# Kernel optimization log

Measured on AMD Instinct MI355X. Metric: run time of the kernel, lower is better.

The kernel has to match this reference:

```python
import jax, jax.numpy as jnp
import numpy as np

C = 64          # channels (init arg)
G = 64          # input latent grid side -> output grid side 2G = 128
S = 2 * G + 2   # padded side for injective key encoding (coords shifted by +1)
N_IN = 60_000


def _encode(coords):
    # injective int32 key for 3D coords in [-1, 2G]
    c = coords + 1
    return (c[:, 0] * S + c[:, 1]) * S + c[:, 2]


def _lookup(keys_sorted, order, query_keys):
    # returns (row index into original arrays, found mask)
    n = keys_sorted.shape[0]
    pos = jnp.clip(jnp.searchsorted(keys_sorted, query_keys), 0, n - 1)
    found = keys_sorted[pos] == query_keys
    return order[pos], found


def _sparse_conv(out_coords, feats, W, b, keys_sorted, order, offsets):
    # Minkowski stride-1 conv: out[i] = sum_k feats[nbr(i, off_k)] @ W[k] + b
    acc = jnp.zeros((out_coords.shape[0], W.shape[-1]), feats.dtype)
    for k in range(offsets.shape[0]):  # 27 fixed kernel offsets
        idx, found = _lookup(keys_sorted, order, _encode(out_coords + offsets[k]))
        nb = jnp.where(found[:, None], feats[idx], jnp.zeros((), feats.dtype))
        acc = acc + nb @ W[k]
    return acc + b


def setup_inputs() -> dict:
    rng = np.random.default_rng(0)
    lin = rng.choice(G ** 3, size=N_IN, replace=False)  # unique occupied voxels
    coords = np.stack([lin // (G * G), (lin // G) % G, lin % G], axis=1).astype(np.int32)
    key = jax.random.key(0)
    ks = jax.random.split(key, 7)
    sc = 0.05
    return {
        'coords': jnp.asarray(coords),
        'feats': jax.random.normal(ks[0], (N_IN, C), jnp.float32),
        'W_up': jax.random.normal(ks[1], (8, C, C), jnp.float32) * sc,
        'b_up': jax.random.normal(ks[2], (C,), jnp.float32) * sc,
        'W1': jax.random.normal(ks[3], (27, C, C), jnp.float32) * sc,
        'b1': jax.random.normal(ks[4], (C,), jnp.float32) * sc,
        'W2': jax.random.normal(ks[5], (27, C, C), jnp.float32) * sc,
        'b2': jax.random.normal(ks[6], (C,), jnp.float32) * sc,
    }


def reference(coords, feats, W_up, b_up, W1, b1, W2, b2):
    # generative transpose conv (kernel 2, stride 2): 8 unique children per voxel
    child = jnp.array([[i, j, k] for i in (0, 1) for j in (0, 1) for k in (0, 1)], jnp.int32)
    out_coords = (2 * coords[:, None, :] + child[None]).reshape(-1, 3)  # [8N, 3]
    x = jnp.einsum('nc,kcd->nkd', feats, W_up).reshape(-1, C) + b_up     # [8N, C]
    x = jax.nn.relu(x)
    # shared kernel-map structure for both stride-1 convs
    keys = _encode(out_coords)
    order = jnp.argsort(keys)
    keys_sorted = keys[order]
    offs = jnp.array([[i, j, k] for i in (-1, 0, 1) for j in (-1, 0, 1) for k in (-1, 0, 1)], jnp.int32)
    x = jax.nn.relu(_sparse_conv(out_coords, x, W1, b1, keys_sorted, order, offs))
    x = _sparse_conv(out_coords, x, W2, b2, keys_sorted, order, offs)
    return x
```

## Files before the change

### kernel.cpp

```cpp
#include <hip/hip_runtime.h>
#include <stdint.h>

typedef __bf16 bf16x8 __attribute__((ext_vector_type(8)));
typedef float f32x4 __attribute__((ext_vector_type(4)));
typedef unsigned short ushort_t;

#define NPARENT 60000
#define NOUT (NPARENT*8)
#define ZIDX NOUT
#define TBL_N (66*66*66)
#define NBIN 4096

static constexpr size_t OFF_TABLE = 0;
static constexpr size_t OFF_CS    = 1152000;
static constexpr size_t OFF_Y     = OFF_CS + 960000;
static constexpr size_t OFF_HIST  = OFF_Y;
static constexpr size_t OFF_CNT   = OFF_Y + 16384;
static constexpr size_t OFF_Z     = OFF_Y + (size_t)(NOUT+1)*128;
static constexpr size_t OFF_FEATB = OFF_Z + (size_t)(NOUT+1)*128;
static constexpr size_t OFF_WUPF  = OFF_FEATB + (size_t)NPARENT*128;
static constexpr size_t OFF_W1F   = OFF_WUPF + (size_t)8*8192;
static constexpr size_t OFF_W2F   = OFF_W1F + (size_t)27*8192;
static constexpr size_t WS_NEED   = OFF_W2F + (size_t)27*8192;

__device__ __forceinline__ ushort_t f2bf(float x) {
  uint32_t u = __float_as_uint(x);
  u += 0x7fffu + ((u >> 16) & 1u);
  return (ushort_t)(u >> 16);
}

__device__ __forceinline__ int binof(int x, int y, int z) {
  int bx = x >> 2, by = y >> 2, bz = z >> 2, m = 0;
  #pragma unroll
  for (int b = 0; b < 4; ++b)
    m |= (((bx>>b)&1) << (3*b+2)) | (((by>>b)&1) << (3*b+1)) | (((bz>>b)&1) << (3*b));
  return m;
}

__device__ __forceinline__ void gl2lds16(const void* g, void* l) {
  __builtin_amdgcn_global_load_lds(
      (const __attribute__((address_space(1))) uint32_t*)g,
      (__attribute__((address_space(3))) uint32_t*)l, 16, 0, 0);
}

__global__ void k_zero(ushort_t* y, ushort_t* z) {
  int t = threadIdx.x;
  if (t < 64) y[(size_t)ZIDX*64 + t] = 0;
  else        z[(size_t)ZIDX*64 + (t-64)] = 0;
}

__global__ void k_hist(const int* __restrict__ coords, int* __restrict__ hist) {
  int i = blockIdx.x*blockDim.x + threadIdx.x;
  if (i >= NPARENT) return;
  atomicAdd(&hist[binof(coords[3*i], coords[3*i+1], coords[3*i+2])], 1);
}

__global__ void k_scan(const int* __restrict__ hist, int* __restrict__ cnt) {
  __shared__ int s[256];
  int t = threadIdx.x;
  int loc[16], sum = 0;
  #pragma unroll
  for (int j=0;j<16;++j){ loc[j]=hist[t*16+j]; sum+=loc[j]; }
  s[t]=sum;
  __syncthreads();
  if (t==0){ int a=0; for (int i=0;i<256;++i){ int v=s[i]; s[i]=a; a+=v; } }
  __syncthreads();
  int a=s[t];
  #pragma unroll
  for (int j=0;j<16;++j){ cnt[t*16+j]=a; a+=loc[j]; }
}

__global__ void k_rank(const int* __restrict__ coords, int* __restrict__ cnt,
                       int4* __restrict__ cs, int* __restrict__ tbl) {
  int i = blockIdx.x*blockDim.x + threadIdx.x;
  if (i >= NPARENT) return;
  int x = coords[3*i], y = coords[3*i+1], z = coords[3*i+2];
  int r = atomicAdd(&cnt[binof(x,y,z)], 1);
  cs[r] = make_int4(x, y, z, i);
  tbl[((x+1)*66 + (y+1))*66 + (z+1)] = r;
}

__global__ void k_feats_bf16(const float4* __restrict__ f, const int4* __restrict__ cs,
                             ushort_t* __restrict__ o, int total) {
  int t = blockIdx.x*blockDim.x + threadIdx.x;
  if (t >= total) return;
  int p = t >> 4, q = t & 15;
  int i = cs[p].w;
  float4 v = f[(size_t)i*16 + q];
  size_t ob = (size_t)p*64 + q*4;
  o[ob+0] = f2bf(v.x); o[ob+1] = f2bf(v.y);
  o[ob+2] = f2bf(v.z); o[ob+3] = f2bf(v.w);
}

__global__ void k_wfrag(const float* __restrict__ w, ushort_t* __restrict__ o, int total) {
  int i = blockIdx.x*blockDim.x + threadIdx.x;
  if (i >= total) return;
  int k = i >> 12, r = i & 4095, c = r >> 6, d = r & 63;
  int nt = d >> 4, lp = d & 15, ks = c >> 5, hi = (c >> 3) & 3, e = c & 7;
  int fi = ks*4 + nt, lane = hi*16 + lp;
  o[(size_t)(k*8 + fi)*512 + lane*8 + e] = f2bf(w[i]);
}

__global__ __launch_bounds__(256) void k_up(const ushort_t* __restrict__ featb,
    const ushort_t* __restrict__ wupf, const float* __restrict__ bup,
    ushort_t* __restrict__ y)
{
  int wave = threadIdx.x >> 6, lane = threadIdx.x & 63;
  int n0 = blockIdx.x*64 + wave*16;
  if (n0 >= NPARENT) return;
  int lp = lane & 15, hi = lane >> 4;
  const ushort_t* ar = featb + (size_t)(n0+lp)*64 + hi*8;
  bf16x8 a0 = *(const bf16x8*)(ar);
  bf16x8 a1 = *(const bf16x8*)(ar + 32);
  float bv[4];
  #pragma unroll
  for (int nt=0; nt<4; ++nt) bv[nt] = bup[nt*16+lp];
  for (int c8=0; c8<8; ++c8) {
    const ushort_t* wb = wupf + (size_t)c8*4096 + lane*8;
    f32x4 acc[4];
    #pragma unroll
    for (int nt=0;nt<4;++nt) acc[nt] = (f32x4){0.f,0.f,0.f,0.f};
    #pragma unroll
    for (int nt=0;nt<4;++nt)
      acc[nt] = __builtin_amdgcn_mfma_f32_16x16x32_bf16(a0, *(const bf16x8*)(wb + nt*512), acc[nt], 0,0,0);
    #pragma unroll
    for (int nt=0;nt<4;++nt)
      acc[nt] = __builtin_amdgcn_mfma_f32_16x16x32_bf16(a1, *(const bf16x8*)(wb + (4+nt)*512), acc[nt], 0,0,0);
    #pragma unroll
    for (int nt=0;nt<4;++nt) {
      #pragma unroll
      for (int j=0;j<4;++j) {
        int par = n0 + hi*4 + j;
        float v = acc[nt][j] + bv[nt];
        v = fmaxf(v, 0.f);
        y[(size_t)(par*8 + c8)*64 + nt*16 + lp] = f2bf(v);
      }
    }
  }
}

template<int RELU, int SCATTER, typename OUT_T>
__global__ __launch_bounds__(256) void k_conv(const int4* __restrict__ cs,
    const int* __restrict__ tbl, const ushort_t* __restrict__ fin,
    const ushort_t* __restrict__ wf, const float* __restrict__ bias,
    OUT_T* __restrict__ out)
{
  __shared__ __align__(16) int nbrs[32*27];
  __shared__ __align__(16) ushort_t bbuf[2][4096];

  int bid = blockIdx.x;
  int xcd = bid & 7, jj = bid >> 3;
  int wg = (xcd < 3 ? xcd*235 : 705 + (xcd-3)*234) + jj;

  int tid = threadIdx.x;
  int wave = tid >> 6, lane = tid & 63;
  int m0 = wg*256 + wave*64;
  int lp = lane & 15, hi = lane >> 4;
  int pblk0 = wg*32;

  for (int i = tid; i < 32*27; i += 256) {
    int p = i / 27, j = i - p*27;
    int4 cc = cs[pblk0 + p];
    int dx = j/9 - 1, dy = (j/3)%3 - 1, dz = j%3 - 1;
    nbrs[i] = tbl[((cc.x+dx+1)*66 + (cc.y+dy+1))*66 + (cc.z+dz+1)];
  }

  {
    const char* wb = (const char*)wf;
    #pragma unroll
    for (int j=0;j<2;++j) {
      int chunk = wave*2 + j;
      gl2lds16(wb + (size_t)chunk*1024 + lane*16, &bbuf[0][chunk*512]);
    }
  }

  int cx = (lp>>2)&1, cy = (lp>>1)&1, cz = lp&1, c = lp&7;
  int plbase = wave*8 + (lp>>3);

  f32x4 acc[4][4];
  #pragma unroll
  for (int s=0;s<4;++s)
    #pragma unroll
    for (int nt=0;nt<4;++nt) acc[s][nt] = (f32x4){0.f,0.f,0.f,0.f};

  const char* finl = (const char*)fin + hi*16;

  __syncthreads();

  #pragma unroll 1
  for (int k=0;k<27;++k) {
    int cur = k & 1;
    int ox = k/9 - 1, oy = (k/3)%3 - 1, oz = k%3 - 1;
    int xk = ((ox&1)<<2) | ((oy&1)<<1) | (oz&1);
    int cpx = c ^ xk;
    uint32_t aoff[4];
    #pragma unroll
    for (int s=0;s<4;++s) {
      int idx = ((cx+ox)>>1)*9 + ((cy+oy)>>1)*3 + ((cz+oz)>>1) + 13;
      int rank = nbrs[(plbase + s*2)*27 + idx];
      uint32_t off = (uint32_t)(rank*8 + cpx) * 128u;
      aoff[s] = (rank < 0) ? (uint32_t)ZIDX*128u : off;
    }
    bf16x8 a[4][2];
    #pragma unroll
    for (int s=0;s<4;++s) {
      a[s][0] = *(const bf16x8*)(finl + aoff[s]);
      a[s][1] = *(const bf16x8*)(finl + aoff[s] + 64);
    }
    if (k < 26) {
      const char* wb = (const char*)wf + (size_t)(k+1)*8192;
      #pragma unroll
      for (int j=0;j<2;++j) {
        int chunk = wave*2 + j;
        gl2lds16(wb + (size_t)chunk*1024 + lane*16, &bbuf[cur^1][chunk*512]);
      }
    }
    bf16x8 bfr[8];
    #pragma unroll
    for (int f=0;f<8;++f) bfr[f] = *(const bf16x8*)&bbuf[cur][f*512 + lane*8];

    #pragma unroll
    for (int s=0;s<4;++s)
      #pragma unroll
      for (int nt=0;nt<4;++nt)
        acc[s][nt] = __builtin_amdgcn_mfma_f32_16x16x32_bf16(a[s][0], bfr[nt], acc[s][nt], 0,0,0);
    #pragma unroll
    for (int s=0;s<4;++s)
      #pragma unroll
      for (int nt=0;nt<4;++nt)
        acc[s][nt] = __builtin_amdgcn_mfma_f32_16x16x32_bf16(a[s][1], bfr[4+nt], acc[s][nt], 0,0,0);

    __syncthreads();
  }

  float bv[4];
  #pragma unroll
  for (int nt=0;nt<4;++nt) bv[nt] = bias[nt*16+lp];
  #pragma unroll
  for (int s=0;s<4;++s) {
    #pragma unroll
    for (int j=0;j<4;++j) {
      int row = m0 + s*16 + hi*4 + j;
      size_t rb;
      if constexpr (SCATTER) {
        int4 cc = cs[row >> 3];
        rb = ((size_t)cc.w*8 + (row & 7)) * 64;
      } else {
        rb = (size_t)row * 64;
      }
      #pragma unroll
      for (int nt=0;nt<4;++nt) {
        float v = acc[s][nt][j] + bv[nt];
        if (RELU) v = fmaxf(v, 0.f);
        size_t oi = rb + nt*16 + lp;
        if constexpr (sizeof(OUT_T)==2) ((ushort_t*)out)[oi] = f2bf(v);
        else                            out[oi] = v;
      }
    }
  }
}

extern "C" void kernel_launch(void* const* d_in, const int* in_sizes, int n_in,
                              void* d_out, int out_size, void* d_ws, size_t ws_size,
                              hipStream_t stream) {
  const int*   coords = (const int*)d_in[0];
  const float* feats  = (const float*)d_in[1];
  const float* Wup    = (const float*)d_in[2];
  const float* bup    = (const float*)d_in[3];
  const float* W1     = (const float*)d_in[4];
  const float* b1     = (const float*)d_in[5];
  const float* W2     = (const float*)d_in[6];
  const float* b2     = (const float*)d_in[7];
  char* ws = (char*)d_ws;
  if (ws_size < WS_NEED) return;

  int*      tbl  = (int*)(ws + OFF_TABLE);
  int4*     cs   = (int4*)(ws + OFF_CS);
  int*      hist = (int*)(ws + OFF_HIST);
  int*      cnt  = (int*)(ws + OFF_CNT);
  ushort_t* y    = (ushort_t*)(ws + OFF_Y);
  ushort_t* z    = (ushort_t*)(ws + OFF_Z);
  ushort_t* fb   = (ushort_t*)(ws + OFF_FEATB);
  ushort_t* wupf = (ushort_t*)(ws + OFF_WUPF);
  ushort_t* w1f  = (ushort_t*)(ws + OFF_W1F);
  ushort_t* w2f  = (ushort_t*)(ws + OFF_W2F);

  hipMemsetAsync(tbl, 0xFF, (size_t)TBL_N*4, stream);
  hipMemsetAsync(hist, 0, (size_t)NBIN*4, stream);
  k_zero<<<1,128,0,stream>>>(y, z);
  k_hist<<<(NPARENT+255)/256,256,0,stream>>>(coords, hist);
  k_scan<<<1,256,0,stream>>>(hist, cnt);
  k_rank<<<(NPARENT+255)/256,256,0,stream>>>(coords, cnt, cs, tbl);
  k_feats_bf16<<<(NPARENT*16+255)/256,256,0,stream>>>((const float4*)feats, cs, fb, NPARENT*16);
  k_wfrag<<<(8*4096+255)/256,256,0,stream>>>(Wup, wupf, 8*4096);
  k_wfrag<<<(27*4096+255)/256,256,0,stream>>>(W1, w1f, 27*4096);
  k_wfrag<<<(27*4096+255)/256,256,0,stream>>>(W2, w2f, 27*4096);
  k_up<<<(NPARENT+63)/64,256,0,stream>>>(fb, wupf, bup, y);
  k_conv<1,0,ushort_t><<<NOUT/256,256,0,stream>>>(cs, tbl, y,  w1f, b1, z);
  k_conv<0,1,float>   <<<NOUT/256,256,0,stream>>>(cs, tbl, z,  w2f, b2, (float*)d_out);
}
```

Baseline: 380.0 us.

## Software-pipeline neighbor gathers and quad-buffer weights in sparse conv kernel

The sparse conv main loop is restructured so that the gather of the next kernel offset's neighbor features is issued before the MFMAs of the current offset. Weights are staged into a 4-deep LDS ring, two offsets ahead, so only one barrier is needed per pair of offsets. The neighbor table is transposed and pre-scaled into byte offsets, with missing neighbors mapped to an 8-row zero pad, so each lane fetches its four offsets with one int4 LDS read and no branch. A launch-bounds hint targets 3 blocks per CU. The cost is more live registers from the double-buffered gather fragments and more LDS, which could limit occupancy.

```diff
diff --git a/kernel.cpp b/kernel.cpp
--- a/kernel.cpp
+++ b/kernel.cpp
@@ -7,17 +7,18 @@
 
 #define NPARENT 60000
 #define NOUT (NPARENT*8)
-#define ZIDX NOUT
+#define ZPB (NPARENT<<10)
 #define TBL_N (66*66*66)
 #define NBIN 4096
 
 static constexpr size_t OFF_TABLE = 0;
-static constexpr size_t OFF_CS    = 1152000;
+static constexpr size_t OFF_CS    = 1149984;
 static constexpr size_t OFF_Y     = OFF_CS + 960000;
 static constexpr size_t OFF_HIST  = OFF_Y;
 static constexpr size_t OFF_CNT   = OFF_Y + 16384;
-static constexpr size_t OFF_Z     = OFF_Y + (size_t)(NOUT+1)*128;
-static constexpr size_t OFF_FEATB = OFF_Z + (size_t)(NOUT+1)*128;
+static constexpr size_t YSZ       = (size_t)(NOUT+8)*128;
+static constexpr size_t OFF_Z     = OFF_Y + YSZ;
+static constexpr size_t OFF_FEATB = OFF_Z + YSZ;
 static constexpr size_t OFF_WUPF  = OFF_FEATB + (size_t)NPARENT*128;
 static constexpr size_t OFF_W1F   = OFF_WUPF + (size_t)8*8192;
 static constexpr size_t OFF_W2F   = OFF_W1F + (size_t)27*8192;
@@ -45,8 +46,8 @@
 
 __global__ void k_zero(ushort_t* y, ushort_t* z) {
   int t = threadIdx.x;
-  if (t < 64) y[(size_t)ZIDX*64 + t] = 0;
-  else        z[(size_t)ZIDX*64 + (t-64)] = 0;
+  if (t < 512) y[(size_t)NOUT*64 + t] = 0;
+  else         z[(size_t)NOUT*64 + (t-512)] = 0;
 }
 
 __global__ void k_hist(const int* __restrict__ coords, int* __restrict__ hist) {
@@ -140,13 +141,13 @@
 }
 
 template<int RELU, int SCATTER, typename OUT_T>
-__global__ __launch_bounds__(256) void k_conv(const int4* __restrict__ cs,
+__global__ __launch_bounds__(256, 3) void k_conv(const int4* __restrict__ cs,
     const int* __restrict__ tbl, const ushort_t* __restrict__ fin,
     const ushort_t* __restrict__ wf, const float* __restrict__ bias,
     OUT_T* __restrict__ out)
 {
-  __shared__ __align__(16) int nbrs[32*27];
-  __shared__ __align__(16) ushort_t bbuf[2][4096];
+  __shared__ __align__(16) int nbt[27*36];
+  __shared__ __align__(16) ushort_t bbuf[4][4096];
 
   int bid = blockIdx.x;
   int xcd = bid & 7, jj = bid >> 3;
@@ -158,24 +159,29 @@
   int lp = lane & 15, hi = lane >> 4;
   int pblk0 = wg*32;
 
-  for (int i = tid; i < 32*27; i += 256) {
-    int p = i / 27, j = i - p*27;
-    int4 cc = cs[pblk0 + p];
+  for (int i = tid; i < 27*32; i += 256) {
+    int j = i >> 5, pi = i & 31;
+    int w = pi >> 3, h = (pi >> 2) & 1, s = pi & 3;
+    int parent = w*8 + s*2 + h;
+    int4 cc = cs[pblk0 + parent];
     int dx = j/9 - 1, dy = (j/3)%3 - 1, dz = j%3 - 1;
-    nbrs[i] = tbl[((cc.x+dx+1)*66 + (cc.y+dy+1))*66 + (cc.z+dz+1)];
-  }
-
-  {
-    const char* wb = (const char*)wf;
-    #pragma unroll
-    for (int j=0;j<2;++j) {
-      int chunk = wave*2 + j;
-      gl2lds16(wb + (size_t)chunk*1024 + lane*16, &bbuf[0][chunk*512]);
+    int r = tbl[((cc.x+dx+1)*66 + (cc.y+dy+1))*66 + (cc.z+dz+1)];
+    nbt[j*36 + pi] = (r < 0 ? NPARENT : r) << 10;
+  }
+
+  #pragma unroll
+  for (int kk=0; kk<2; ++kk) {
+    const char* wb = (const char*)wf + (size_t)kk*8192;
+    #pragma unroll
+    for (int j2=0;j2<2;++j2) {
+      int chunk = wave*2 + j2;
+      gl2lds16(wb + chunk*1024 + lane*16, &bbuf[kk][chunk*512]);
     }
   }
 
   int cx = (lp>>2)&1, cy = (lp>>1)&1, cz = lp&1, c = lp&7;
-  int plbase = wave*8 + (lp>>3);
+  int evbase = wave*32 + (lp>>3)*16;
+  const char* finl = (const char*)fin + hi*16;
 
   f32x4 acc[4][4];
   #pragma unroll
@@ -183,55 +189,67 @@
     #pragma unroll
     for (int nt=0;nt<4;++nt) acc[s][nt] = (f32x4){0.f,0.f,0.f,0.f};
 
-  const char* finl = (const char*)fin + hi*16;
-
-  __syncthreads();
-
-  #pragma unroll 1
-  for (int k=0;k<27;++k) {
-    int cur = k & 1;
+  auto prefetch = [&](int k, int* voff, bf16x8* gp) {
     int ox = k/9 - 1, oy = (k/3)%3 - 1, oz = k%3 - 1;
     int xk = ((ox&1)<<2) | ((oy&1)<<1) | (oz&1);
-    int cpx = c ^ xk;
-    uint32_t aoff[4];
-    #pragma unroll
-    for (int s=0;s<4;++s) {
-      int idx = ((cx+ox)>>1)*9 + ((cy+oy)>>1)*3 + ((cz+oz)>>1) + 13;
-      int rank = nbrs[(plbase + s*2)*27 + idx];
-      uint32_t off = (uint32_t)(rank*8 + cpx) * 128u;
-      aoff[s] = (rank < 0) ? (uint32_t)ZIDX*128u : off;
+    int cpxoff = (c ^ xk) << 7;
+    int idx = ((cx+ox)>>1)*9 + ((cy+oy)>>1)*3 + ((cz+oz)>>1) + 13;
+    int4 ev = *(const int4*)((const char*)nbt + idx*144 + evbase);
+    voff[0] = ev.x + cpxoff; voff[1] = ev.y + cpxoff;
+    voff[2] = ev.z + cpxoff; voff[3] = ev.w + cpxoff;
+    #pragma unroll
+    for (int s=0;s<4;++s) gp[s] = *(const bf16x8*)(finl + voff[s]);
+  };
+
+  auto stage = [&](int k) {
+    const char* wb = (const char*)wf + (size_t)k*8192;
+    #pragma unroll
+    for (int j2=0;j2<2;++j2) {
+      int chunk = wave*2 + j2;
+      gl2lds16(wb + chunk*1024 + lane*16, &bbuf[k&3][chunk*512]);
     }
-    bf16x8 a[4][2];
-    #pragma unroll
-    for (int s=0;s<4;++s) {
-      a[s][0] = *(const bf16x8*)(finl + aoff[s]);
-      a[s][1] = *(const bf16x8*)(finl + aoff[s] + 64);
-    }
-    if (k < 26) {
-      const char* wb = (const char*)wf + (size_t)(k+1)*8192;
-      #pragma unroll
-      for (int j=0;j<2;++j) {
-        int chunk = wave*2 + j;
-        gl2lds16(wb + (size_t)chunk*1024 + lane*16, &bbuf[cur^1][chunk*512]);
-      }
-    }
-    bf16x8 bfr[8];
-    #pragma unroll
-    for (int f=0;f<8;++f) bfr[f] = *(const bf16x8*)&bbuf[cur][f*512 + lane*8];
-
+  };
+
+  auto consume = [&](int k, const int* voff, const bf16x8* gp) {
+    const ushort_t* bb = &bbuf[k&3][0];
+    bf16x8 g2[4];
+    #pragma unroll
+    for (int s=0;s<4;++s) g2[s] = *(const bf16x8*)(finl + voff[s] + 64);
+    bf16x8 b0[4];
+    #pragma unroll
+    for (int f=0;f<4;++f) b0[f] = *(const bf16x8*)&bb[f*512 + lane*8];
     #pragma unroll
     for (int s=0;s<4;++s)
       #pragma unroll
       for (int nt=0;nt<4;++nt)
-        acc[s][nt] = __builtin_amdgcn_mfma_f32_16x16x32_bf16(a[s][0], bfr[nt], acc[s][nt], 0,0,0);
+        acc[s][nt] = __builtin_amdgcn_mfma_f32_16x16x32_bf16(gp[s], b0[nt], acc[s][nt], 0,0,0);
+    bf16x8 b1[4];
+    #pragma unroll
+    for (int f=0;f<4;++f) b1[f] = *(const bf16x8*)&bb[(4+f)*512 + lane*8];
     #pragma unroll
     for (int s=0;s<4;++s)
       #pragma unroll
       for (int nt=0;nt<4;++nt)
-        acc[s][nt] = __builtin_amdgcn_mfma_f32_16x16x32_bf16(a[s][1], bfr[4+nt], acc[s][nt], 0,0,0);
-
+        acc[s][nt] = __builtin_amdgcn_mfma_f32_16x16x32_bf16(g2[s], b1[nt], acc[s][nt], 0,0,0);
+  };
+
+  __syncthreads();
+
+  int voffA[4], voffB[4];
+  bf16x8 gpA[4], gpB[4];
+  prefetch(0, voffA, gpA);
+
+  #pragma unroll 1
+  for (int kp = 0; kp < 26; kp += 2) {
+    stage(kp+2);
+    prefetch(kp+1, voffB, gpB);
+    consume(kp, voffA, gpA);
+    if (kp+3 < 27) stage(kp+3);
+    prefetch(kp+2, voffA, gpA);
+    consume(kp+1, voffB, gpB);
     __syncthreads();
   }
+  consume(26, voffA, gpA);
 
   float bv[4];
   #pragma unroll
@@ -287,10 +305,10 @@
 
   hipMemsetAsync(tbl, 0xFF, (size_t)TBL_N*4, stream);
   hipMemsetAsync(hist, 0, (size_t)NBIN*4, stream);
-  k_zero<<<1,128,0,stream>>>(y, z);
   k_hist<<<(NPARENT+255)/256,256,0,stream>>>(coords, hist);
   k_scan<<<1,256,0,stream>>>(hist, cnt);
   k_rank<<<(NPARENT+255)/256,256,0,stream>>>(coords, cnt, cs, tbl);
+  k_zero<<<1,1024,0,stream>>>(y, z);
   k_feats_bf16<<<(NPARENT*16+255)/256,256,0,stream>>>((const float4*)feats, cs, fb, NPARENT*16);
   k_wfrag<<<(8*4096+255)/256,256,0,stream>>>(Wup, wupf, 8*4096);
   k_wfrag<<<(27*4096+255)/256,256,0,stream>>>(W1, w1f, 27*4096);
```

Result: slower. 485.3 us (+27.7%).
